# Optimization experiments

Hardware: AMD Instinct MI355X
Metric: run time of the kernel (lower is better)

Reference implementation:

```python
import jax, jax.numpy as jnp
import numpy as np

D_MODEL = 2048
NHEADS = 16
NOPE = 128
ROPE = 64
VDIM = 128
QLORA = 1536
KVLORA = 512
QHD = NOPE + ROPE  # 192
B, T = 1, 4096


def rms_norm(x, w):
    # torch.nn.RMSNorm with eps=None uses finfo(dtype).eps
    eps = jnp.finfo(x.dtype).eps
    var = jnp.mean(x * x, axis=-1, keepdims=True)
    return x * jax.lax.rsqrt(var + eps) * w


def rope_cos_sin(T, dim):
    freqs = 1.0 / (10000.0 ** (jnp.arange(0, dim, 2, dtype=jnp.float32) / dim))
    ang = jnp.arange(T, dtype=jnp.float32)[:, None] * freqs[None, :]  # (T, dim/2)
    return jnp.cos(ang), jnp.sin(ang)


def apply_rope(x, cos, sin):
    # interleaved RoPE: even/odd channel pairs rotated
    xe = x[..., 0::2]
    xo = x[..., 1::2]
    re = xe * cos - xo * sin
    ro = xo * cos + xe * sin
    return jnp.stack([re, ro], axis=-1).reshape(x.shape)


def setup_inputs() -> dict:
    key = jax.random.key(0)
    ks = jax.random.split(key, 6)
    s = 0.02
    return {
        "x": jax.random.normal(ks[0], (B, T, D_MODEL), jnp.float32),
        "Wqa": jax.random.normal(ks[1], (D_MODEL, QLORA), jnp.float32) * s,
        "q_ln_w": jnp.ones((QLORA,), jnp.float32),
        "Wqb": jax.random.normal(ks[2], (QLORA, NHEADS * QHD), jnp.float32) * s,
        "Wkva": jax.random.normal(ks[3], (D_MODEL, KVLORA + ROPE), jnp.float32) * s,
        "kv_ln_w": jnp.ones((KVLORA,), jnp.float32),
        "Wkvb": jax.random.normal(ks[4], (KVLORA, NHEADS * (NOPE + VDIM)), jnp.float32) * s,
        "Wo": jax.random.normal(ks[5], (NHEADS * VDIM, D_MODEL), jnp.float32) * s,
    }


def reference(x, Wqa, q_ln_w, Wqb, Wkva, kv_ln_w, Wkvb, Wo):
    Bx, Tx, _ = x.shape
    cos, sin = rope_cos_sin(Tx, ROPE)  # (T, ROPE/2)

    # Low-rank Q path
    q = rms_norm(x @ Wqa, q_ln_w) @ Wqb
    q = q.reshape(Bx, Tx, NHEADS, QHD).transpose(0, 2, 1, 3)  # (B,H,T,QHD)
    q_nope = q[..., :NOPE]
    q_rope = apply_rope(q[..., NOPE:], cos, sin)  # (B,H,T,ROPE)

    # Compressed KV path + shared rope key
    kv = x @ Wkva
    kv_c = kv[..., :KVLORA]  # (B,T,KVLORA) latent cache
    k_rope = apply_rope(kv[..., KVLORA:], cos, sin)  # (B,T,ROPE), head-shared

    kvb = (rms_norm(kv_c, kv_ln_w) @ Wkvb).reshape(Bx, Tx, NHEADS, NOPE + VDIM)
    k_nope = kvb[..., :NOPE].transpose(0, 2, 1, 3)  # (B,H,T,NOPE)
    v = kvb[..., NOPE:].transpose(0, 2, 1, 3)       # (B,H,T,VDIM)

    # Scores split into nope part + head-shared rope part (avoids expanding k_rope to H heads)
    scale = 1.0 / jnp.sqrt(jnp.float32(QHD))
    s = jnp.einsum('bhqd,bhkd->bhqk', q_nope, k_nope)
    s = s + jnp.einsum('bhqd,bkd->bhqk', q_rope, k_rope)
    s = s * scale

    mask = jnp.tril(jnp.ones((Tx, Tx), dtype=bool))
    s = jnp.where(mask, s, -jnp.inf)
    a = jax.nn.softmax(s, axis=-1)

    o = jnp.einsum('bhqk,bhkd->bhqd', a, v)
    o = o.transpose(0, 2, 1, 3).reshape(Bx, Tx, NHEADS * VDIM)
    return o @ Wo
```

## Files before the change

kernel.cpp:

```cpp
#include <hip/hip_runtime.h>
#include <hip/hip_bf16.h>

typedef __attribute__((ext_vector_type(8))) short short8;
typedef __attribute__((ext_vector_type(4))) float f32x4;

#define GLDS16(gp, lp)                                                         \
  __builtin_amdgcn_global_load_lds(                                            \
      (const __attribute__((address_space(1))) void*)(gp),                     \
      (__attribute__((address_space(3))) void*)(lp), 16, 0, 0)

static __device__ __forceinline__ unsigned int pack_bf16(float a, float b) {
  __hip_bfloat16 ba = __float2bfloat16(a), bb = __float2bfloat16(b);
  unsigned short ua = *reinterpret_cast<unsigned short*>(&ba);
  unsigned short ub = *reinterpret_cast<unsigned short*>(&bb);
  return (unsigned int)ua | ((unsigned int)ub << 16);
}

static __device__ __forceinline__ int xcd_swz(int linear, int nwg) {
  return (linear & 7) * (nwg >> 3) + (linear >> 3);
}

__global__ __launch_bounds__(256) void cast_tr_kernel(
    const float* __restrict__ x, __hip_bfloat16* __restrict__ x_bf,
    const float* __restrict__ Wqa, const float* __restrict__ Wkva,
    __hip_bfloat16* __restrict__ WdownT,
    float* __restrict__ cs, float* __restrict__ sn)
{
  __shared__ float tile[32][33];
  int b = blockIdx.x;
  const int tid = threadIdx.x;
  if (b < 8192) {
    int i = b * 256 + tid;
    float4 v = ((const float4*)x)[i];
    x_bf[(size_t)i * 4 + 0] = __float2bfloat16(v.x);
    x_bf[(size_t)i * 4 + 1] = __float2bfloat16(v.y);
    x_bf[(size_t)i * 4 + 2] = __float2bfloat16(v.z);
    x_bf[(size_t)i * 4 + 3] = __float2bfloat16(v.w);
    if (b < 4096 && tid < 32) {
      float freq = powf(10000.f, -2.f * (float)tid / 64.f);
      float ang = (float)b * freq;
      cs[b * 32 + tid] = cosf(ang);
      sn[b * 32 + tid] = sinf(ang);
    }
    return;
  }
  b -= 8192;
  const float* in;
  __hip_bfloat16* outp;
  int K, N, Npad, gx;
  if (b < 3072) { in = Wqa;  outp = WdownT;                        K = 2048; N = 1536; Npad = 1536; gx = 48; }
  else { b -= 3072; in = Wkva; outp = WdownT + (size_t)1536 * 2048; K = 2048; N = 576;  Npad = 640;  gx = 20; }
  int n0 = (b % gx) * 32, k0 = (b / gx) * 32;
  int tx = tid & 31, ty = tid >> 5;
  #pragma unroll
  for (int i = ty; i < 32; i += 8) {
    int k = k0 + i, n = n0 + tx;
    tile[i][tx] = (n < N) ? in[(size_t)k * N + n] : 0.f;
  }
  __syncthreads();
  #pragma unroll
  for (int i = ty; i < 32; i += 8) {
    int n = n0 + i, k = k0 + tx;
    if (n < Npad) outp[(size_t)n * K + k] = __float2bfloat16(tile[tx][i]);
  }
}

#define GEMM128_CORE(A, BT, Kdim)                                              \
  const int wave = tid >> 6, lane = tid & 63;                                  \
  const int wr = wave >> 1, wc = wave & 1;                                     \
  const int lq = lane & 15, grp = lane >> 4;                                   \
  const f32x4 z4 = {0.f, 0.f, 0.f, 0.f};                                       \
  f32x4 acc[4][4];                                                             \
  _Pragma("unroll") for (int i = 0; i < 4; i++)                                \
      _Pragma("unroll") for (int j = 0; j < 4; j++) acc[i][j] = z4;            \
  for (int k0 = 0; k0 < (Kdim); k0 += 32) {                                    \
    _Pragma("unroll") for (int i = 0; i < 2; i++) {                            \
      const int t = wave + 4 * i;                                              \
      const int c = t * 64 + lane;                                             \
      const int cr = c >> 2;                                                   \
      const int ko = (c & 3) << 3;                                             \
      GLDS16((A) + (size_t)(row0 + cr) * (Kdim) + (k0 + ko), (char*)As + t * 1024); \
      GLDS16((BT) + (size_t)(col0 + cr) * (Kdim) + (k0 + ko), (char*)Bs + t * 1024);\
    }                                                                          \
    __syncthreads();                                                           \
    short8 af[4], bfr[4];                                                      \
    _Pragma("unroll") for (int mm = 0; mm < 4; mm++)                           \
      af[mm] = *(const short8*)((const short*)As + ((wr * 64 + mm * 16 + lq) * 32 + grp * 8)); \
    _Pragma("unroll") for (int nn = 0; nn < 4; nn++)                           \
      bfr[nn] = *(const short8*)((const short*)Bs + ((wc * 64 + nn * 16 + lq) * 32 + grp * 8));\
    _Pragma("unroll") for (int mm = 0; mm < 4; mm++)                           \
      _Pragma("unroll") for (int nn = 0; nn < 4; nn++)                         \
        acc[mm][nn] = __builtin_amdgcn_mfma_f32_16x16x32_bf16(af[mm], bfr[nn], acc[mm][nn], 0, 0, 0); \
    __syncthreads();                                                           \
  }

__global__ __launch_bounds__(256) void gemm_bt_kernel(
    const __hip_bfloat16* __restrict__ A,
    const __hip_bfloat16* __restrict__ BT,
    float* __restrict__ C, int M, int N, int K)
{
  __shared__ __hip_bfloat16 As[128 * 32];
  __shared__ __hip_bfloat16 Bs[128 * 32];
  const int tid = threadIdx.x;
  const int nwg = gridDim.x * gridDim.y;
  const int orig = xcd_swz(blockIdx.y * gridDim.x + blockIdx.x, nwg);
  const int row0 = (orig / gridDim.x) * 128;
  const int col0 = (orig % gridDim.x) * 128;
  GEMM128_CORE(A, BT, K)
  (void)M;
  #pragma unroll
  for (int mm = 0; mm < 4; mm++)
    #pragma unroll
    for (int nn = 0; nn < 4; nn++) {
      const int row = row0 + wr * 64 + mm * 16 + grp * 4;
      const int col = col0 + wc * 64 + nn * 16 + lq;
      float* Cp = C + (size_t)row * N + col;
      #pragma unroll
      for (int rr = 0; rr < 4; rr++) Cp[(size_t)rr * N] = acc[mm][nn][rr];
    }
}

__global__ __launch_bounds__(256) void gemm_down_tr_kernel(
    const __hip_bfloat16* __restrict__ A,
    const __hip_bfloat16* __restrict__ BT,
    float* __restrict__ q_lat, float* __restrict__ kvout,
    const float* __restrict__ Wqb, const float* __restrict__ Wkvb,
    const float* __restrict__ Wo,
    __hip_bfloat16* __restrict__ WqbT, __hip_bfloat16* __restrict__ WkvbT,
    __hip_bfloat16* __restrict__ WoT)
{
  __shared__ __align__(16) char smem[16512];
  const int tid = threadIdx.x;
  int b = blockIdx.x;
  if (b < 544) {
    __hip_bfloat16* As = (__hip_bfloat16*)smem;
    __hip_bfloat16* Bs = (__hip_bfloat16*)(smem + 8192);
    const int orig = xcd_swz(b, 544);
    const int row0 = (orig / 17) * 128;
    const int col0 = (orig % 17) * 128;
    GEMM128_CORE(A, BT, 2048)
    #pragma unroll
    for (int mm = 0; mm < 4; mm++)
      #pragma unroll
      for (int nn = 0; nn < 4; nn++) {
        const int row = row0 + wr * 64 + mm * 16 + grp * 4;
        const int col = col0 + wc * 64 + nn * 16 + lq;
        float* Cp = (col < 1536) ? (q_lat + (size_t)row * 1536 + col)
                                 : (kvout + (size_t)row * 640 + (col - 1536));
        const size_t ld = (col < 1536) ? 1536 : 640;
        #pragma unroll
        for (int rr = 0; rr < 4; rr++) Cp[(size_t)rr * ld] = acc[mm][nn][rr];
      }
    return;
  }
  b -= 544;
  float (*tile)[33] = (float(*)[33])smem;
  const float* in;
  __hip_bfloat16* outp;
  int K, N, Npad, gx;
  if (b < 4608)      { in = Wqb;  outp = WqbT;  K = 1536; N = 3072; Npad = 3072; gx = 96; }
  else if (b < 6656) { b -= 4608; in = Wkvb; outp = WkvbT; K = 512;  N = 4096; Npad = 4096; gx = 128; }
  else               { b -= 6656; in = Wo;   outp = WoT;   K = 2048; N = 2048; Npad = 2048; gx = 64; }
  int n0 = (b % gx) * 32, k0 = (b / gx) * 32;
  int tx = tid & 31, ty = tid >> 5;
  #pragma unroll
  for (int i = ty; i < 32; i += 8) {
    int k = k0 + i, n = n0 + tx;
    tile[i][tx] = (n < N) ? in[(size_t)k * N + n] : 0.f;
  }
  __syncthreads();
  #pragma unroll
  for (int i = ty; i < 32; i += 8) {
    int n = n0 + i, k = k0 + tx;
    if (n < Npad) outp[(size_t)n * K + k] = __float2bfloat16(tile[tx][i]);
  }
}

#define GEMM256_MAIN(Aptr, BTptr, Kdim)                                        \
  __shared__ __align__(16) char Ab[2][32768];                                  \
  __shared__ __align__(16) char Bb[2][32768];                                  \
  const int tid = threadIdx.x;                                                 \
  const int wid = tid >> 6, lane = tid & 63;                                   \
  const int wm = wid >> 2, wn = wid & 3;                                       \
  const int lq = lane & 15, grp = lane >> 4;                                   \
  const int nwg = gridDim.x * gridDim.y;                                       \
  const int orig = xcd_swz(blockIdx.y * gridDim.x + blockIdx.x, nwg);          \
  const int row0 = (orig / gridDim.x) * 256;                                   \
  const int col0 = (orig % gridDim.x) * 256;                                   \
  const size_t K2 = (size_t)(Kdim) * 2;                                        \
  const char* pa[4]; const char* pb[4]; int ldst[4];                           \
  _Pragma("unroll") for (int i = 0; i < 4; i++) {                              \
    int L = i * 8192 + tid * 16;                                               \
    int r = L >> 7;                                                            \
    int csw = (L & 127) ^ ((r & 7) << 4);                                      \
    ldst[i] = L;                                                               \
    pa[i] = (const char*)(Aptr) + (size_t)(row0 + r) * K2 + csw;               \
    pb[i] = (const char*)(BTptr) + (size_t)(col0 + r) * K2 + csw;              \
  }                                                                            \
  const int xm = (lq & 7) << 4;                                                \
  const f32x4 z4 = {0.f, 0.f, 0.f, 0.f};                                       \
  f32x4 acc[8][4];                                                             \
  _Pragma("unroll") for (int i = 0; i < 8; i++)                                \
    _Pragma("unroll") for (int j = 0; j < 4; j++) acc[i][j] = z4;              \
  const int nt = (Kdim) >> 6;                                                  \
  _Pragma("unroll") for (int i = 0; i < 4; i++) {                              \
    GLDS16(pa[i], &Ab[0][0] + ldst[i]);                                        \
    GLDS16(pb[i], &Bb[0][0] + ldst[i]);                                        \
  }                                                                            \
  for (int t = 0; t < nt; ++t) {                                               \
    const int b = t & 1;                                                       \
    if (t + 1 < nt) {                                                          \
      const size_t koff = (size_t)(t + 1) * 128;                               \
      _Pragma("unroll") for (int i = 0; i < 4; i++) {                          \
        GLDS16(pa[i] + koff, &Ab[b ^ 1][0] + ldst[i]);                         \
        GLDS16(pb[i] + koff, &Bb[b ^ 1][0] + ldst[i]);                         \
      }                                                                        \
      asm volatile("s_waitcnt vmcnt(8)" ::: "memory");                         \
    } else {                                                                   \
      asm volatile("s_waitcnt vmcnt(0)" ::: "memory");                         \
    }                                                                          \
    __builtin_amdgcn_sched_barrier(0);                                         \
    __builtin_amdgcn_s_barrier();                                              \
    __builtin_amdgcn_sched_barrier(0);                                         \
    const char* Ar = &Ab[b][0];                                                \
    const char* Br = &Bb[b][0];                                                \
    short8 bfr[4][2];                                                          \
    _Pragma("unroll") for (int n = 0; n < 4; n++)                              \
      _Pragma("unroll") for (int ks = 0; ks < 2; ks++)                         \
        bfr[n][ks] = *(const short8*)(Br + (wn * 64 + n * 16 + lq) * 128 +     \
                                      ((ks * 64 + grp * 16) ^ xm));            \
    _Pragma("unroll") for (int mh = 0; mh < 4; mh++) {                         \
      short8 af[2][2];                                                         \
      _Pragma("unroll") for (int mi = 0; mi < 2; mi++)                         \
        _Pragma("unroll") for (int ks = 0; ks < 2; ks++)                       \
          af[mi][ks] = *(const short8*)(Ar + (wm * 128 + (mh * 2 + mi) * 16 + lq) * 128 + \
                                        ((ks * 64 + grp * 16) ^ xm));          \
      __builtin_amdgcn_s_setprio(1);                                           \
      _Pragma("unroll") for (int mi = 0; mi < 2; mi++)                         \
        _Pragma("unroll") for (int n = 0; n < 4; n++)                          \
          _Pragma("unroll") for (int ks = 0; ks < 2; ks++)                     \
            acc[mh * 2 + mi][n] = __builtin_amdgcn_mfma_f32_16x16x32_bf16(     \
                af[mi][ks], bfr[n][ks], acc[mh * 2 + mi][n], 0, 0, 0);         \
      __builtin_amdgcn_s_setprio(0);                                           \
    }                                                                          \
    __builtin_amdgcn_sched_barrier(0);                                         \
    __builtin_amdgcn_s_barrier();                                              \
    __builtin_amdgcn_sched_barrier(0);                                         \
  }

__global__ __launch_bounds__(512, 2) void gemm256_qup_kernel(
    const __hip_bfloat16* __restrict__ A,
    const __hip_bfloat16* __restrict__ BT,
    __hip_bfloat16* __restrict__ Qh,
    const float* __restrict__ cs_tab, const float* __restrict__ sn_tab, int K)
{
  GEMM256_MAIN(A, BT, K)
  const float scale = 0.10411654209f;
  #pragma unroll
  for (int m = 0; m < 8; m++)
    #pragma unroll
    for (int n = 0; n < 4; n++) {
      const int col = col0 + wn * 64 + n * 16 + lq;
      const int h = col / 192;
      const int d = col - h * 192;
      const bool is_rope = (d >= 128);
      const int i = (d - 128) >> 1;
      const float sgn = (d & 1) ? 1.f : -1.f;
      #pragma unroll
      for (int rr = 0; rr < 4; rr++) {
        const int t = row0 + wm * 128 + m * 16 + grp * 4 + rr;
        float val = acc[m][n][rr];
        float partner = __shfl_xor(val, 1);
        float outv = val;
        if (is_rope) {
          float c = cs_tab[t * 32 + i];
          float s = sn_tab[t * 32 + i];
          outv = val * c + sgn * partner * s;
        }
        Qh[((size_t)h * 4096 + t) * 192 + d] = __float2bfloat16(outv * scale);
      }
    }
}

__global__ __launch_bounds__(512, 2) void gemm256_kvup_kernel(
    const __hip_bfloat16* __restrict__ A,
    const __hip_bfloat16* __restrict__ BT,
    __hip_bfloat16* __restrict__ Kh,
    __hip_bfloat16* __restrict__ Vt, int K)
{
  GEMM256_MAIN(A, BT, K)
  #pragma unroll
  for (int m = 0; m < 8; m++)
    #pragma unroll
    for (int n = 0; n < 4; n++) {
      const int col = col0 + wn * 64 + n * 16 + lq;
      const int h = col >> 8;
      const int j = col & 255;
      const int t0 = row0 + wm * 128 + m * 16 + grp * 4;
      if (j < 128) {
        #pragma unroll
        for (int rr = 0; rr < 4; rr++)
          Kh[((size_t)h * 4096 + t0 + rr) * 192 + j] = __float2bfloat16(acc[m][n][rr]);
      } else {
        const int vd = j - 128;
        uint2 w;
        w.x = pack_bf16(acc[m][n][0], acc[m][n][1]);
        w.y = pack_bf16(acc[m][n][2], acc[m][n][3]);
        *(uint2*)(Vt + ((size_t)h * 128 + vd) * 4096 + t0) = w;
      }
    }
}

__global__ __launch_bounds__(256) void rmsnorm2_kernel(
    const float* __restrict__ q_lat, const float* __restrict__ kv,
    const float* __restrict__ qw, const float* __restrict__ kvw,
    __hip_bfloat16* __restrict__ q_ln, __hip_bfloat16* __restrict__ kv_ln,
    const float* __restrict__ cs_tab, const float* __restrict__ sn_tab,
    __hip_bfloat16* __restrict__ Kh)
{
  const int b = blockIdx.x;
  const bool isq = (b < 4096);
  const int row = isq ? b : b - 4096;
  const int ld = isq ? 1536 : 640;
  const int W = isq ? 1536 : 512;
  const float* x = (isq ? q_lat : kv) + (size_t)row * ld;
  const float* w = isq ? qw : kvw;
  __hip_bfloat16* out = (isq ? q_ln : kv_ln) + (size_t)row * W;
  const int tid = threadIdx.x;
  const int wave = tid >> 6, lane = tid & 63;
  float ss = 0.f;
  for (int i = tid; i < W; i += 256) { float v = x[i]; ss += v * v; }
  #pragma unroll
  for (int o = 32; o; o >>= 1) ss += __shfl_xor(ss, o);
  __shared__ float red[4];
  __shared__ float stot;
  if (lane == 0) red[wave] = ss;
  __syncthreads();
  if (tid == 0) stot = red[0] + red[1] + red[2] + red[3];
  __syncthreads();
  const float rstd = rsqrtf(stot / (float)W + 1.1920929e-7f);
  for (int i = tid; i < W; i += 256)
    out[i] = __float2bfloat16(x[i] * rstd * w[i]);
  if (!isq) {
    const int t = row;
    for (int e = tid; e < 512; e += 256) {
      int h = e >> 5, i = e & 31;
      float c = cs_tab[t * 32 + i], s = sn_tab[t * 32 + i];
      float xe = x[512 + 2 * i];
      float xo = x[512 + 2 * i + 1];
      size_t base = ((size_t)h * 4096 + t) * 192 + 128 + 2 * i;
      Kh[base]     = __float2bfloat16(xe * c - xo * s);
      Kh[base + 1] = __float2bfloat16(xo * c + xe * s);
    }
  }
}

__global__ __launch_bounds__(256, 2) void flash_attn_kernel(
    const __hip_bfloat16* __restrict__ Qh,
    const __hip_bfloat16* __restrict__ Kh,
    const __hip_bfloat16* __restrict__ Vt,
    __hip_bfloat16* __restrict__ Obf)
{
  __shared__ __align__(16) char Klds[2][24576];
  __shared__ __align__(16) char Vlds[2][16384];

  const int hw = blockIdx.x;
  const int rest = hw >> 3;
  const int h = (hw & 7) + 8 * (rest & 1);
  const int p = rest >> 1;

  const int wave = threadIdx.x >> 6;
  const int lane = threadIdx.x & 63;
  const int lq = lane & 15;
  const int grp = lane >> 4;
  const int qb_[2] = {(63 - p) * 64 + wave * 16,
                      p * 64 + wave * 16};
  const int kendA = qb_[0] + 16;
  const int kendB = qb_[1] + 16;
  const int nt = 64 - p;

  const char* Kh_ = (const char*)(Kh + (size_t)h * 4096 * 192);
  const char* Vh_ = (const char*)(Vt + (size_t)h * 128 * 4096);
  const short* Qh_ = (const short*)Qh + (size_t)h * 4096 * 192;

  int kbase[6], vbase[4];
  #pragma unroll
  for (int i = 0; i < 6; i++) {
    int L = (wave * 6 + i) * 1024 + lane * 16;
    int r = L / 384, c = L - r * 384;
    int swb = (r & 3) | (((r >> 3) & 1) << 2);
    kbase[i] = r * 384 + (c ^ (swb << 4));
  }
  #pragma unroll
  for (int i = 0; i < 4; i++) {
    int L = (wave * 4 + i) * 1024 + lane * 16;
    int r = L >> 7, c = L & 127;
    vbase[i] = r * 8192 + (c ^ ((r & 7) << 4));
  }

  short8 qf[2][6];
  #pragma unroll
  for (int f = 0; f < 2; f++)
    #pragma unroll
    for (int d = 0; d < 6; d++)
      qf[f][d] = *(const short8*)(Qh_ + (size_t)(qb_[f] + lq) * 192 + d * 32 + grp * 8);

  const f32x4 z4 = {0.f, 0.f, 0.f, 0.f};
  f32x4 o_acc[2][8];
  #pragma unroll
  for (int f = 0; f < 2; f++)
    #pragma unroll
    for (int v = 0; v < 8; v++) o_acc[f][v] = z4;
  float m[2] = {-1e30f, -1e30f};
  float lsum[2] = {0.f, 0.f};

  const int krow_l = ((lq >> 2) << 3) + (lq & 3);
  const int kxm = ((lq & 3) | (((lq >> 2) & 1) << 2)) << 4;
  const int vxm = (lq & 7) << 4;

  {
    #pragma unroll
    for (int i = 0; i < 6; i++) GLDS16(Kh_ + kbase[i], Klds[0] + (wave * 6 + i) * 1024);
    #pragma unroll
    for (int i = 0; i < 4; i++) GLDS16(Vh_ + vbase[i], Vlds[0] + (wave * 4 + i) * 1024);
  }

  for (int t = 0; t < nt; t++) {
    __syncthreads();
    if (t + 1 < nt) {
      const char* Kp = Kh_ + (size_t)(t + 1) * 64 * 384;
      const char* Vp = Vh_ + (size_t)(t + 1) * 128;
      char* Kd = Klds[(t + 1) & 1];
      char* Vd = Vlds[(t + 1) & 1];
      #pragma unroll
      for (int i = 0; i < 6; i++) GLDS16(Kp + kbase[i], Kd + (wave * 6 + i) * 1024);
      #pragma unroll
      for (int i = 0; i < 4; i++) GLDS16(Vp + vbase[i], Vd + (wave * 4 + i) * 1024);
    }
    const char* Kb = Klds[t & 1];
    const char* Vb = Vlds[t & 1];
    const int ks = t * 64;

    #pragma unroll
    for (int h2 = 0; h2 < 2; h2++) {
      const int ks32 = ks + h2 * 32;
      if (ks32 >= kendA) continue;
      const bool act1 = (ks32 < kendB);

      f32x4 st[2][2];
      #pragma unroll
      for (int kt = 0; kt < 2; kt++) {
        const int row = h2 * 32 + krow_l + kt * 4;
        short8 kf[6];
        #pragma unroll
        for (int d = 0; d < 6; d++)
          kf[d] = *(const short8*)(Kb + row * 384 + ((d * 64 + grp * 16) ^ kxm));
        __builtin_amdgcn_s_setprio(1);
        #pragma unroll
        for (int f = 0; f < 2; f++) {
          if (f == 1 && !act1) continue;
          f32x4 acc = z4;
          #pragma unroll
          for (int d = 0; d < 6; d++)
            acc = __builtin_amdgcn_mfma_f32_16x16x32_bf16(kf[d], qf[f][d], acc, 0, 0, 0);
          st[f][kt] = acc;
        }
        __builtin_amdgcn_s_setprio(0);
      }

      short8 vf[8];
      #pragma unroll
      for (int v = 0; v < 8; v++)
        vf[v] = *(const short8*)(Vb + (v * 16 + lq) * 128 + ((h2 * 64 + grp * 16) ^ vxm));

      #pragma unroll
      for (int f = 0; f < 2; f++) {
        if (f == 1 && !act1) continue;
        const int qg = qb_[f] + lq;
        const bool need_mask = (ks32 + 31 > qb_[f]);
        if (need_mask) {
          #pragma unroll
          for (int kt = 0; kt < 2; kt++)
            #pragma unroll
            for (int r = 0; r < 4; r++) {
              int key = ks32 + grp * 8 + kt * 4 + r;
              if (key > qg) st[f][kt][r] = -1e30f;
            }
        }
        float tmax = fmaxf(fmaxf(fmaxf(st[f][0][0], st[f][0][1]), fmaxf(st[f][0][2], st[f][0][3])),
                           fmaxf(fmaxf(st[f][1][0], st[f][1][1]), fmaxf(st[f][1][2], st[f][1][3])));
        tmax = fmaxf(tmax, __shfl_xor(tmax, 16));
        tmax = fmaxf(tmax, __shfl_xor(tmax, 32));
        if (!__all(tmax <= m[f] + 11.5416f)) {
          float mnew = fmaxf(m[f], tmax);
          float alpha = exp2f(m[f] - mnew);
          m[f] = mnew;
          lsum[f] *= alpha;
          float a0 = __shfl(alpha, grp * 4 + 0);
          float a1 = __shfl(alpha, grp * 4 + 1);
          float a2 = __shfl(alpha, grp * 4 + 2);
          float a3 = __shfl(alpha, grp * 4 + 3);
          #pragma unroll
          for (int v = 0; v < 8; v++) {
            o_acc[f][v][0] *= a0; o_acc[f][v][1] *= a1;
            o_acc[f][v][2] *= a2; o_acc[f][v][3] *= a3;
          }
        }
        float p00 = exp2f(st[f][0][0] - m[f]), p01 = exp2f(st[f][0][1] - m[f]);
        float p02 = exp2f(st[f][0][2] - m[f]), p03 = exp2f(st[f][0][3] - m[f]);
        float p10 = exp2f(st[f][1][0] - m[f]), p11 = exp2f(st[f][1][1] - m[f]);
        float p12 = exp2f(st[f][1][2] - m[f]), p13 = exp2f(st[f][1][3] - m[f]);
        lsum[f] += ((p00 + p01) + (p02 + p03)) + ((p10 + p11) + (p12 + p13));
        union { unsigned int u[4]; short8 s8; } pu;
        pu.u[0] = pack_bf16(p00, p01);
        pu.u[1] = pack_bf16(p02, p03);
        pu.u[2] = pack_bf16(p10, p11);
        pu.u[3] = pack_bf16(p12, p13);
        short8 pa = pu.s8;
        __builtin_amdgcn_s_setprio(1);
        #pragma unroll
        for (int v = 0; v < 8; v++)
          o_acc[f][v] = __builtin_amdgcn_mfma_f32_16x16x32_bf16(pa, vf[v], o_acc[f][v], 0, 0, 0);
        __builtin_amdgcn_s_setprio(0);
      }
    }
  }

  #pragma unroll
  for (int f = 0; f < 2; f++) {
    float ls = lsum[f];
    ls += __shfl_xor(ls, 16);
    ls += __shfl_xor(ls, 32);
    float linv = 1.f / ls;
    float l0 = __shfl(linv, grp * 4 + 0);
    float l1 = __shfl(linv, grp * 4 + 1);
    float l2 = __shfl(linv, grp * 4 + 2);
    float l3 = __shfl(linv, grp * 4 + 3);
    const int qb = qb_[f];
    #pragma unroll
    for (int v = 0; v < 8; v++) {
      int col = h * 128 + v * 16 + lq;
      Obf[(size_t)(qb + grp * 4 + 0) * 2048 + col] = __float2bfloat16(o_acc[f][v][0] * l0);
      Obf[(size_t)(qb + grp * 4 + 1) * 2048 + col] = __float2bfloat16(o_acc[f][v][1] * l1);
      Obf[(size_t)(qb + grp * 4 + 2) * 2048 + col] = __float2bfloat16(o_acc[f][v][2] * l2);
      Obf[(size_t)(qb + grp * 4 + 3) * 2048 + col] = __float2bfloat16(o_acc[f][v][3] * l3);
    }
  }
}

extern "C" void kernel_launch(void* const* d_in, const int* in_sizes, int n_in,
                              void* d_out, int out_size, void* d_ws, size_t ws_size,
                              hipStream_t stream)
{
  (void)in_sizes; (void)n_in; (void)out_size; (void)ws_size;
  const float* x     = (const float*)d_in[0];
  const float* Wqa   = (const float*)d_in[1];
  const float* qlnw  = (const float*)d_in[2];
  const float* Wqb   = (const float*)d_in[3];
  const float* Wkva  = (const float*)d_in[4];
  const float* kvlnw = (const float*)d_in[5];
  const float* Wkvb  = (const float*)d_in[6];
  const float* Wo    = (const float*)d_in[7];
  float* out = (float*)d_out;
  char* ws = (char*)d_ws;

  size_t off = 0;
  auto take = [&](size_t bytes) {
    char* p = ws + off;
    off += (bytes + 255) & ~(size_t)255;
    return p;
  };

  __hip_bfloat16* x_bf   = (__hip_bfloat16*)take((size_t)4096 * 2048 * 2);
  __hip_bfloat16* WdownT = (__hip_bfloat16*)take((size_t)2176 * 2048 * 2);
  __hip_bfloat16* WqbT   = (__hip_bfloat16*)take((size_t)3072 * 1536 * 2);
  __hip_bfloat16* WkvbT  = (__hip_bfloat16*)take((size_t)4096 * 512 * 2);
  __hip_bfloat16* WoT    = (__hip_bfloat16*)take((size_t)2048 * 2048 * 2);
  char* regA             = take((size_t)4096 * 1536 * 4);
  float* kv              = (float*)take((size_t)4096 * 640 * 4);
  __hip_bfloat16* q_ln   = (__hip_bfloat16*)take((size_t)4096 * 1536 * 2);
  __hip_bfloat16* kv_ln  = (__hip_bfloat16*)take((size_t)4096 * 512 * 2);
  float* cs_tab          = (float*)take((size_t)4096 * 32 * 4);
  float* sn_tab          = (float*)take((size_t)4096 * 32 * 4);
  __hip_bfloat16* Khp    = (__hip_bfloat16*)take((size_t)16 * 4096 * 192 * 2);
  __hip_bfloat16* Vtp    = (__hip_bfloat16*)take((size_t)16 * 128 * 4096 * 2);
  __hip_bfloat16* o_bf   = (__hip_bfloat16*)take((size_t)4096 * 2048 * 2);

  float* q_lat = (float*)regA;
  __hip_bfloat16* Qh = (__hip_bfloat16*)regA;

  cast_tr_kernel<<<dim3(12544), 256, 0, stream>>>(x, x_bf, Wqa, Wkva, WdownT,
                                                  cs_tab, sn_tab);

  gemm_down_tr_kernel<<<dim3(11296), 256, 0, stream>>>(
      x_bf, WdownT, q_lat, kv, Wqb, Wkvb, Wo, WqbT, WkvbT, WoT);

  rmsnorm2_kernel<<<dim3(8192), 256, 0, stream>>>(q_lat, kv, qlnw, kvlnw, q_ln, kv_ln,
                                                  cs_tab, sn_tab, Khp);

  gemm256_qup_kernel<<<dim3(12, 16), 512, 0, stream>>>(q_ln, WqbT, Qh, cs_tab, sn_tab, 1536);
  gemm256_kvup_kernel<<<dim3(16, 16), 512, 0, stream>>>(kv_ln, WkvbT, Khp, Vtp, 512);

  flash_attn_kernel<<<dim3(512), 256, 0, stream>>>(Qh, Khp, Vtp, o_bf);

  gemm_bt_kernel<<<dim3(16, 32), 256, 0, stream>>>(o_bf, WoT, out, 4096, 2048, 2048);
}
```

Before: 433.9 us.

## Switch up-projection and output GEMMs to 256x128 tiles with double-buffered LDS

Replaces the 256x256 tile GEMM macro with a 256x128 variant (8 waves as 4x2, each computing 64x64) and uses it for the Q-up, KV-up, and output projections. The Q-up and KV-up grids double in block count to fill more CUs. The old 128x128 single-buffer output GEMM is replaced by the pipelined swizzled-LDS kernel. This trades lower per-block reuse for better occupancy and wave balance across the GPU.

Result: slower. 445.1 us (+2.6%).

```diff
diff --git a/kernel.cpp b/kernel.cpp
--- a/kernel.cpp
+++ b/kernel.cpp
@@ -94,32 +94,6 @@
     __syncthreads();                                                           \
   }
 
-__global__ __launch_bounds__(256) void gemm_bt_kernel(
-    const __hip_bfloat16* __restrict__ A,
-    const __hip_bfloat16* __restrict__ BT,
-    float* __restrict__ C, int M, int N, int K)
-{
-  __shared__ __hip_bfloat16 As[128 * 32];
-  __shared__ __hip_bfloat16 Bs[128 * 32];
-  const int tid = threadIdx.x;
-  const int nwg = gridDim.x * gridDim.y;
-  const int orig = xcd_swz(blockIdx.y * gridDim.x + blockIdx.x, nwg);
-  const int row0 = (orig / gridDim.x) * 128;
-  const int col0 = (orig % gridDim.x) * 128;
-  GEMM128_CORE(A, BT, K)
-  (void)M;
-  #pragma unroll
-  for (int mm = 0; mm < 4; mm++)
-    #pragma unroll
-    for (int nn = 0; nn < 4; nn++) {
-      const int row = row0 + wr * 64 + mm * 16 + grp * 4;
-      const int col = col0 + wc * 64 + nn * 16 + lq;
-      float* Cp = C + (size_t)row * N + col;
-      #pragma unroll
-      for (int rr = 0; rr < 4; rr++) Cp[(size_t)rr * N] = acc[mm][nn][rr];
-    }
-}
-
 __global__ __launch_bounds__(256) void gemm_down_tr_kernel(
     const __hip_bfloat16* __restrict__ A,
     const __hip_bfloat16* __restrict__ BT,
@@ -176,46 +150,50 @@
   }
 }
 
-#define GEMM256_MAIN(Aptr, BTptr, Kdim)                                        \
-  __shared__ __align__(16) char Ab[2][32768];                                  \
-  __shared__ __align__(16) char Bb[2][32768];                                  \
+#define GEMM256x128_MAIN(Aptr, BTptr, Kdim)                                    \
+  __shared__ __align__(16) char Ab[2][32768];             \
+  __shared__ __align__(16) char Bb[2][16384];             \
   const int tid = threadIdx.x;                                                 \
   const int wid = tid >> 6, lane = tid & 63;                                   \
-  const int wm = wid >> 2, wn = wid & 3;                                       \
+  const int wm = wid >> 1, wn = wid & 1;                                       \
   const int lq = lane & 15, grp = lane >> 4;                                   \
   const int nwg = gridDim.x * gridDim.y;                                       \
   const int orig = xcd_swz(blockIdx.y * gridDim.x + blockIdx.x, nwg);          \
   const int row0 = (orig / gridDim.x) * 256;                                   \
-  const int col0 = (orig % gridDim.x) * 256;                                   \
+  const int col0 = (orig % gridDim.x) * 128;                                   \
   const size_t K2 = (size_t)(Kdim) * 2;                                        \
-  const char* pa[4]; const char* pb[4]; int ldst[4];                           \
+  const char* pa[4]; const char* pb[2]; int ldstA[4], ldstB[2];                \
   _Pragma("unroll") for (int i = 0; i < 4; i++) {                              \
     int L = i * 8192 + tid * 16;                                               \
     int r = L >> 7;                                                            \
     int csw = (L & 127) ^ ((r & 7) << 4);                                      \
-    ldst[i] = L;                                                               \
+    ldstA[i] = L;                                                              \
     pa[i] = (const char*)(Aptr) + (size_t)(row0 + r) * K2 + csw;               \
+  }                                                                            \
+  _Pragma("unroll") for (int i = 0; i < 2; i++) {                              \
+    int L = i * 8192 + tid * 16;                                               \
+    int r = L >> 7;                                                            \
+    int csw = (L & 127) ^ ((r & 7) << 4);                                      \
+    ldstB[i] = L;                                                              \
     pb[i] = (const char*)(BTptr) + (size_t)(col0 + r) * K2 + csw;              \
   }                                                                            \
   const int xm = (lq & 7) << 4;                                                \
   const f32x4 z4 = {0.f, 0.f, 0.f, 0.f};                                       \
-  f32x4 acc[8][4];                                                             \
-  _Pragma("unroll") for (int i = 0; i < 8; i++)                                \
+  f32x4 acc[4][4];                                                             \
+  _Pragma("unroll") for (int i = 0; i < 4; i++)                                \
     _Pragma("unroll") for (int j = 0; j < 4; j++) acc[i][j] = z4;              \
   const int nt = (Kdim) >> 6;                                                  \
-  _Pragma("unroll") for (int i = 0; i < 4; i++) {                              \
-    GLDS16(pa[i], &Ab[0][0] + ldst[i]);                                        \
-    GLDS16(pb[i], &Bb[0][0] + ldst[i]);                                        \
-  }                                                                            \
+  _Pragma("unroll") for (int i = 0; i < 4; i++) GLDS16(pa[i], &Ab[0][0] + ldstA[i]); \
+  _Pragma("unroll") for (int i = 0; i < 2; i++) GLDS16(pb[i], &Bb[0][0] + ldstB[i]); \
   for (int t = 0; t < nt; ++t) {                                               \
     const int b = t & 1;                                                       \
     if (t + 1 < nt) {                                                          \
       const size_t koff = (size_t)(t + 1) * 128;                               \
-      _Pragma("unroll") for (int i = 0; i < 4; i++) {                          \
-        GLDS16(pa[i] + koff, &Ab[b ^ 1][0] + ldst[i]);                         \
-        GLDS16(pb[i] + koff, &Bb[b ^ 1][0] + ldst[i]);                         \
-      }                                                                        \
-      asm volatile("s_waitcnt vmcnt(8)" ::: "memory");                         \
+      _Pragma("unroll") for (int i = 0; i < 4; i++)                            \
+        GLDS16(pa[i] + koff, &Ab[b ^ 1][0] + ldstA[i]);                        \
+      _Pragma("unroll") for (int i = 0; i < 2; i++)                            \
+        GLDS16(pb[i] + koff, &Bb[b ^ 1][0] + ldstB[i]);                        \
+      asm volatile("s_waitcnt vmcnt(6)" ::: "memory");                         \
     } else {                                                                   \
       asm volatile("s_waitcnt vmcnt(0)" ::: "memory");                         \
     }                                                                          \
@@ -224,40 +202,55 @@
     __builtin_amdgcn_sched_barrier(0);                                         \
     const char* Ar = &Ab[b][0];                                                \
     const char* Br = &Bb[b][0];                                                \
-    short8 bfr[4][2];                                                          \
+    short8 bfr[4][2], af[4][2];                                                \
     _Pragma("unroll") for (int n = 0; n < 4; n++)                              \
       _Pragma("unroll") for (int ks = 0; ks < 2; ks++)                         \
         bfr[n][ks] = *(const short8*)(Br + (wn * 64 + n * 16 + lq) * 128 +     \
                                       ((ks * 64 + grp * 16) ^ xm));            \
-    _Pragma("unroll") for (int mh = 0; mh < 4; mh++) {                         \
-      short8 af[2][2];                                                         \
-      _Pragma("unroll") for (int mi = 0; mi < 2; mi++)                         \
+    _Pragma("unroll") for (int m = 0; m < 4; m++)                              \
+      _Pragma("unroll") for (int ks = 0; ks < 2; ks++)                         \
+        af[m][ks] = *(const short8*)(Ar + (wm * 64 + m * 16 + lq) * 128 +      \
+                                     ((ks * 64 + grp * 16) ^ xm));             \
+    __builtin_amdgcn_s_setprio(1);                                             \
+    _Pragma("unroll") for (int m = 0; m < 4; m++)                              \
+      _Pragma("unroll") for (int n = 0; n < 4; n++)                            \
         _Pragma("unroll") for (int ks = 0; ks < 2; ks++)                       \
-          af[mi][ks] = *(const short8*)(Ar + (wm * 128 + (mh * 2 + mi) * 16 + lq) * 128 + \
-                                        ((ks * 64 + grp * 16) ^ xm));          \
-      __builtin_amdgcn_s_setprio(1);                                           \
-      _Pragma("unroll") for (int mi = 0; mi < 2; mi++)                         \
-        _Pragma("unroll") for (int n = 0; n < 4; n++)                          \
-          _Pragma("unroll") for (int ks = 0; ks < 2; ks++)                     \
-            acc[mh * 2 + mi][n] = __builtin_amdgcn_mfma_f32_16x16x32_bf16(     \
-                af[mi][ks], bfr[n][ks], acc[mh * 2 + mi][n], 0, 0, 0);         \
-      __builtin_amdgcn_s_setprio(0);                                           \
-    }                                                                          \
+          acc[m][n] = __builtin_amdgcn_mfma_f32_16x16x32_bf16(                 \
+              af[m][ks], bfr[n][ks], acc[m][n], 0, 0, 0);                      \
+    __builtin_amdgcn_s_setprio(0);                                             \
     __builtin_amdgcn_sched_barrier(0);                                         \
     __builtin_amdgcn_s_barrier();                                              \
     __builtin_amdgcn_sched_barrier(0);                                         \
   }
 
-__global__ __launch_bounds__(512, 2) void gemm256_qup_kernel(
+__global__ __launch_bounds__(512, 1) void gemmw_bt_kernel(
+    const __hip_bfloat16* __restrict__ A,
+    const __hip_bfloat16* __restrict__ BT,
+    float* __restrict__ C, int N, int K)
+{
+  GEMM256x128_MAIN(A, BT, K)
+  #pragma unroll
+  for (int m = 0; m < 4; m++)
+    #pragma unroll
+    for (int n = 0; n < 4; n++) {
+      const int row = row0 + wm * 64 + m * 16 + grp * 4;
+      const int col = col0 + wn * 64 + n * 16 + lq;
+      float* Cp = C + (size_t)row * N + col;
+      #pragma unroll
+      for (int rr = 0; rr < 4; rr++) Cp[(size_t)rr * N] = acc[m][n][rr];
+    }
+}
+
+__global__ __launch_bounds__(512, 1) void gemmw_qup_kernel(
     const __hip_bfloat16* __restrict__ A,
     const __hip_bfloat16* __restrict__ BT,
     __hip_bfloat16* __restrict__ Qh,
     const float* __restrict__ cs_tab, const float* __restrict__ sn_tab, int K)
 {
-  GEMM256_MAIN(A, BT, K)
+  GEMM256x128_MAIN(A, BT, K)
   const float scale = 0.10411654209f;
   #pragma unroll
-  for (int m = 0; m < 8; m++)
+  for (int m = 0; m < 4; m++)
     #pragma unroll
     for (int n = 0; n < 4; n++) {
       const int col = col0 + wn * 64 + n * 16 + lq;
@@ -268,7 +261,7 @@
       const float sgn = (d & 1) ? 1.f : -1.f;
       #pragma unroll
       for (int rr = 0; rr < 4; rr++) {
-        const int t = row0 + wm * 128 + m * 16 + grp * 4 + rr;
+        const int t = row0 + wm * 64 + m * 16 + grp * 4 + rr;
         float val = acc[m][n][rr];
         float partner = __shfl_xor(val, 1);
         float outv = val;
@@ -282,21 +275,21 @@
     }
 }
 
-__global__ __launch_bounds__(512, 2) void gemm256_kvup_kernel(
+__global__ __launch_bounds__(512, 1) void gemmw_kvup_kernel(
     const __hip_bfloat16* __restrict__ A,
     const __hip_bfloat16* __restrict__ BT,
     __hip_bfloat16* __restrict__ Kh,
     __hip_bfloat16* __restrict__ Vt, int K)
 {
-  GEMM256_MAIN(A, BT, K)
-  #pragma unroll
-  for (int m = 0; m < 8; m++)
+  GEMM256x128_MAIN(A, BT, K)
+  #pragma unroll
+  for (int m = 0; m < 4; m++)
     #pragma unroll
     for (int n = 0; n < 4; n++) {
       const int col = col0 + wn * 64 + n * 16 + lq;
       const int h = col >> 8;
       const int j = col & 255;
-      const int t0 = row0 + wm * 128 + m * 16 + grp * 4;
+      const int t0 = row0 + wm * 64 + m * 16 + grp * 4;
       if (j < 128) {
         #pragma unroll
         for (int rr = 0; rr < 4; rr++)
@@ -598,10 +591,10 @@
   rmsnorm2_kernel<<<dim3(8192), 256, 0, stream>>>(q_lat, kv, qlnw, kvlnw, q_ln, kv_ln,
                                                   cs_tab, sn_tab, Khp);
 
-  gemm256_qup_kernel<<<dim3(12, 16), 512, 0, stream>>>(q_ln, WqbT, Qh, cs_tab, sn_tab, 1536);
-  gemm256_kvup_kernel<<<dim3(16, 16), 512, 0, stream>>>(kv_ln, WkvbT, Khp, Vtp, 512);
+  gemmw_qup_kernel<<<dim3(24, 16), 512, 0, stream>>>(q_ln, WqbT, Qh, cs_tab, sn_tab, 1536);
+  gemmw_kvup_kernel<<<dim3(32, 16), 512, 0, stream>>>(kv_ln, WkvbT, Khp, Vtp, 512);
 
   flash_attn_kernel<<<dim3(512), 256, 0, stream>>>(Qh, Khp, Vtp, o_bf);
 
-  gemm_bt_kernel<<<dim3(16, 32), 256, 0, stream>>>(o_bf, WoT, out, 4096, 2048, 2048);
-}
+  gemmw_bt_kernel<<<dim3(16, 16), 512, 0, stream>>>(o_bf, WoT, out, 2048, 2048);
+}
```
